# Kernel optimization log

Measured on AMD Instinct MI355X. Metric: run time of the kernel, lower is better.

Reference implementation:

```python
import jax, jax.numpy as jnp
import numpy as np

WBITS = 4
GROUP_SIZE = 64
QMAX = 2 ** WBITS - 1  # 15
EPS = 1e-5


def setup_inputs() -> dict:
    key = jax.random.key(0)
    k1, k2, k3 = jax.random.split(key, 3)
    x = jax.random.normal(k1, (1, 512, 11008), dtype=jnp.float32)
    weight = jax.random.normal(k2, (4096, 11008), dtype=jnp.float32) * 0.02
    bias = jax.random.normal(k3, (4096,), dtype=jnp.float32) * 0.02
    return {"x": x, "weight": weight, "bias": bias}


def fake_quant_groupwise(w: jnp.ndarray) -> jnp.ndarray:
    """Uniform affine (asymmetric) group-wise fake quantization of the weight.

    Groups of GROUP_SIZE contiguous elements along the flattened weight share
    one (scale, zero_point) pair, computed dynamically from min/max per group,
    as in UniformAffineQuantizer(wbits, group_size, weight).
    """
    orig_shape = w.shape
    wg = w.reshape(-1, GROUP_SIZE)                     # [n_groups, G]
    xmin = jnp.min(wg, axis=1, keepdims=True)          # [n_groups, 1]
    xmax = jnp.max(wg, axis=1, keepdims=True)
    scale = jnp.maximum(xmax - xmin, EPS) / QMAX       # [n_groups, 1]
    zero_point = jnp.round(-xmin / scale)              # [n_groups, 1]
    w_int = jnp.clip(jnp.round(wg / scale) + zero_point, 0, QMAX)
    w_dq = (w_int - zero_point) * scale
    return w_dq.reshape(orig_shape)


def reference(x, weight, bias):
    w_q = fake_quant_groupwise(weight)                 # [out, in]
    # F.linear: x @ w_q.T + bias
    out = jnp.einsum('bsi,oi->bso', x, w_q) + bias
    return out
```

## Files before the change

kernel.cpp:

```cpp
#include <hip/hip_runtime.h>
#include <hip/hip_bf16.h>
#include <stdint.h>

typedef __attribute__((ext_vector_type(8))) short bf16x8;
typedef __attribute__((ext_vector_type(8))) short short8;
typedef __attribute__((ext_vector_type(4))) float f32x4;

#define M_DIM 512
#define N_DIM 4096
#define K_DIM 11008
#define KSTEPS 172

#define GLOBAL_AS(p) ((const __attribute__((address_space(1))) void*)(p))
#define LDS_AS(p)    ((__attribute__((address_space(3))) void*)(p))

__device__ __forceinline__ short f2bf(float f) {
    unsigned u = __float_as_uint(f);
    unsigned r = u + 0x7fff + ((u >> 16) & 1);
    return (short)(r >> 16);
}

__device__ __forceinline__ unsigned cvt_pk_bf16(float lo, float hi) {
    unsigned r;
    asm("v_cvt_pk_bf16_f32 %0, %1, %2" : "=v"(r) : "v"(lo), "v"(hi));
    return r;
}

__device__ __forceinline__ float dpp_xor1(float v) {
    return __int_as_float(__builtin_amdgcn_mov_dpp(__float_as_int(v), 0xB1, 0xf, 0xf, true));
}
__device__ __forceinline__ float dpp_xor2(float v) {
    return __int_as_float(__builtin_amdgcn_mov_dpp(__float_as_int(v), 0x4E, 0xf, 0xf, true));
}

__device__ __forceinline__ void fence_bar() {
    asm volatile("" ::: "memory");
    __builtin_amdgcn_s_barrier();
    asm volatile("" ::: "memory");
}
#define LGKM0() asm volatile("s_waitcnt lgkmcnt(0)" ::: "memory")
#define VMCNT(n) asm volatile("s_waitcnt vmcnt(" #n ")" ::: "memory")

__global__ __launch_bounds__(256) void conv_x(const float* __restrict__ x, short* __restrict__ xb) {
    const long long total = (long long)M_DIM * K_DIM;
    for (long long e0 = ((long long)blockIdx.x * 256 + threadIdx.x) * 8;
         e0 < total;
         e0 += (long long)gridDim.x * 256 * 8) {
        const float4* p = (const float4*)(x + e0);
        float4 v0 = p[0];
        float4 v1 = p[1];
        short8 s;
        s[0] = f2bf(v0.x); s[1] = f2bf(v0.y); s[2] = f2bf(v0.z); s[3] = f2bf(v0.w);
        s[4] = f2bf(v1.x); s[5] = f2bf(v1.y); s[6] = f2bf(v1.z); s[7] = f2bf(v1.w);
        *(short8*)(xb + e0) = s;
    }
}

__global__ __launch_bounds__(256, 2) void gemm_fq(const short* __restrict__ A,
                                                  const float* __restrict__ W,
                                                  unsigned short* __restrict__ P,
                                                  int spb) {
    __shared__ short As[2][256 * 64];
    __shared__ short Bs[128 * 64];
    const int tid  = threadIdx.x;
    const int lane = tid & 63;
    const int w    = tid >> 6;
    const int wr   = w >> 1;
    const int wc   = w & 1;
    const int m0   = blockIdx.y * 256;
    const int n0   = blockIdx.x * 128;
    const int kt0  = blockIdx.z * spb;
    const int kt1  = min(kt0 + spb, KSTEPS);

    const int srow = lane >> 3;
    const int sswz = (lane & 7) ^ srow;
    const int rC   = tid >> 2;
    const int qC   = tid & 3;
    const int arow = wr * 128 + (lane & 15);
    const int brow = wc * 64 + (lane & 15);
    const int qb   = lane >> 4;

    f32x4  acc[8][4] = {};
    float4 C0[4], C1[4];

    auto stageA = [&](int d, int kt) {
        #pragma unroll
        for (int i = 0; i < 8; ++i) {
            const int rb = w * 64 + i * 8;
            __builtin_amdgcn_global_load_lds(
                GLOBAL_AS(A + (size_t)(m0 + rb + srow) * K_DIM + kt * 64 + sswz * 8),
                LDS_AS(&As[d][rb * 64]), 16, 0, 0);
        }
    };
    auto loadC = [&](float4 (&dst)[4], int c, int kt) {
        const float4* src = (const float4*)(W + (size_t)(n0 + c * 64 + rC) * K_DIM + (size_t)kt * 64 + qC * 16);
        #pragma unroll
        for (int j = 0; j < 4; ++j) dst[j] = src[j];
    };
    auto quantC = [&](const float4 (&v)[4], int c) {
        const float* pv = (const float*)&v[0];
        float mns[8], mxs[8];
        #pragma unroll
        for (int j = 0; j < 8; ++j) {
            mns[j] = fminf(pv[2 * j], pv[2 * j + 1]);
            mxs[j] = fmaxf(pv[2 * j], pv[2 * j + 1]);
        }
        #pragma unroll
        for (int st = 4; st >= 1; st >>= 1)
            #pragma unroll
            for (int j = 0; j < st; ++j) {
                mns[j] = fminf(mns[j], mns[j + st]);
                mxs[j] = fmaxf(mxs[j], mxs[j + st]);
            }
        float mn = fminf(mns[0], dpp_xor1(mns[0]));
        mn = fminf(mn, dpp_xor2(mn));
        float mx = fmaxf(mxs[0], dpp_xor1(mxs[0]));
        mx = fmaxf(mx, dpp_xor2(mx));
        float range = fmaxf(mx - mn, 1e-5f);
        float scale = range * (1.0f / 15.0f);
        float rs    = 1.0f / scale;
        const int r    = c * 64 + rC;
        const int base = r * 64;
        #pragma unroll
        for (int s4 = 0; s4 < 2; ++s4) {
            float q[8];
            #pragma unroll
            for (int j = 0; j < 8; ++j)
                q[j] = rintf(pv[s4 * 8 + j] * rs) * scale;
            union { unsigned u[4]; short8 s; } pk;
            #pragma unroll
            for (int j = 0; j < 4; ++j)
                pk.u[j] = cvt_pk_bf16(q[2 * j], q[2 * j + 1]);
            const int s = qC * 2 + s4;
            *(short8*)&Bs[base + ((s ^ (r & 7)) * 8)] = pk.s;
        }
    };

    loadC(C0, 0, kt0);
    loadC(C1, 1, kt0);
    stageA(0, kt0);
    VMCNT(12); quantC(C0, 0);
    VMCNT(8);  quantC(C1, 1);
    loadC(C0, 0, kt0 + 1);
    loadC(C1, 1, kt0 + 1);
    VMCNT(8);
    LGKM0();
    fence_bar();

    int par = 0;
    for (int t = kt0; t < kt1; ++t) {
        const int tn  = (t + 1 < kt1) ? t + 1 : t;
        const int tn2 = (t + 2 < kt1) ? t + 2 : kt1 - 1;
        const short* Asc = As[par];

        stageA(par ^ 1, tn);

        bf16x8 bfr[2][4];
        #pragma unroll
        for (int ks = 0; ks < 2; ++ks)
            #pragma unroll
            for (int fn = 0; fn < 4; ++fn) {
                const int r = brow + fn * 16;
                bfr[ks][fn] = *(const bf16x8*)&Bs[r * 64 + (((ks * 4 + qb) ^ (r & 7)) * 8)];
            }
        #pragma unroll
        for (int qd = 0; qd < 4; ++qd) {
            bf16x8 af[2][2];
            #pragma unroll
            for (int ks = 0; ks < 2; ++ks)
                #pragma unroll
                for (int j = 0; j < 2; ++j) {
                    const int r = arow + (qd * 2 + j) * 16;
                    af[ks][j] = *(const bf16x8*)&Asc[r * 64 + (((ks * 4 + qb) ^ (r & 7)) * 8)];
                }
            #pragma unroll
            for (int ks = 0; ks < 2; ++ks)
                #pragma unroll
                for (int j = 0; j < 2; ++j)
                    #pragma unroll
                    for (int fn = 0; fn < 4; ++fn)
                        acc[qd * 2 + j][fn] = __builtin_amdgcn_mfma_f32_16x16x32_bf16(
                            af[ks][j], bfr[ks][fn], acc[qd * 2 + j][fn], 0, 0, 0);
        }
        fence_bar();

        VMCNT(12);
        quantC(C0, 0);
        VMCNT(8);
        quantC(C1, 1);
        loadC(C0, 0, tn2);
        loadC(C1, 1, tn2);
        VMCNT(8);
        LGKM0();
        fence_bar();
        par ^= 1;
    }

    VMCNT(0);

    unsigned short* out = P + (size_t)blockIdx.z * M_DIM * N_DIM;
    #pragma unroll
    for (int fm = 0; fm < 8; ++fm) {
        #pragma unroll
        for (int fn = 0; fn < 4; ++fn) {
            const int col  = n0 + wc * 64 + fn * 16 + (lane & 15);
            const int rowb = m0 + wr * 128 + fm * 16 + (lane >> 4) * 4;
            #pragma unroll
            for (int r = 0; r < 4; ++r) {
                out[(size_t)(rowb + r) * N_DIM + col] = (unsigned short)f2bf(acc[fm][fn][r]);
            }
        }
    }
}

__global__ __launch_bounds__(256) void reduce_out(const unsigned short* __restrict__ P,
                                                  const float* __restrict__ bias,
                                                  float* __restrict__ out,
                                                  int splitk) {
    const size_t total = (size_t)M_DIM * N_DIM;
    for (size_t idx8 = ((size_t)blockIdx.x * 256 + threadIdx.x) * 8;
         idx8 < total;
         idx8 += (size_t)gridDim.x * 256 * 8) {
        const int col = (int)(idx8 % N_DIM);
        float s[8];
        {
            float4 b0 = *(const float4*)(bias + col);
            float4 b1 = *(const float4*)(bias + col + 4);
            s[0] = b0.x; s[1] = b0.y; s[2] = b0.z; s[3] = b0.w;
            s[4] = b1.x; s[5] = b1.y; s[6] = b1.z; s[7] = b1.w;
        }
        for (int sp = 0; sp < splitk; ++sp) {
            short8 p = *(const short8*)(P + (size_t)sp * total + idx8);
            #pragma unroll
            for (int j = 0; j < 8; ++j)
                s[j] += __uint_as_float(((unsigned)(unsigned short)p[j]) << 16);
        }
        float4 o0 = {s[0], s[1], s[2], s[3]};
        float4 o1 = {s[4], s[5], s[6], s[7]};
        *(float4*)(out + idx8) = o0;
        *(float4*)(out + idx8 + 4) = o1;
    }
}

extern "C" void kernel_launch(void* const* d_in, const int* in_sizes, int n_in,
                              void* d_out, int out_size, void* d_ws, size_t ws_size,
                              hipStream_t stream) {
    const float* x    = (const float*)d_in[0];
    const float* wgt  = (const float*)d_in[1];
    const float* bias = (const float*)d_in[2];
    float* out = (float*)d_out;

    char* ws = (char*)d_ws;
    const size_t xb_bytes = (size_t)M_DIM * K_DIM * 2;
    short* xb = (short*)ws;
    unsigned short* part = (unsigned short*)(ws + xb_bytes);

    const size_t per_split = (size_t)M_DIM * N_DIM * 2;
    size_t avail = (ws_size > xb_bytes) ? (ws_size - xb_bytes) : 0;
    int splitk = 1, spb = KSTEPS;
    for (int sk = 8; sk >= 1; --sk) {
        if ((size_t)sk * per_split > avail) continue;
        int s = (KSTEPS + sk - 1) / sk;
        int last = KSTEPS - (sk - 1) * s;
        if (last < 2) continue;
        splitk = sk; spb = s;
        break;
    }

    hipLaunchKernelGGL(conv_x, dim3(2048), dim3(256), 0, stream, x, xb);
    hipLaunchKernelGGL(gemm_fq, dim3(N_DIM / 128, M_DIM / 256, splitk), dim3(256), 0, stream,
                       xb, wgt, part, spb);
    hipLaunchKernelGGL(reduce_out, dim3(1024), dim3(256), 0, stream, part, bias, out, splitk);
}
```

Baseline: 87.97 us.

## Double GEMM block to 512 threads, halving per-wave accumulator tiles

The GEMM block grows from 4 to 8 waves while keeping the same 256x128 output tile. Each wave now computes a 64x64 subtile with half the accumulators, and each thread loads and quantizes one 64-float weight group instead of two. The inner loop is reordered to load B fragments per k-substep. The aim is lower register pressure and more waves to hide latency, at the cost of fewer MFMAs per LDS read and heavier barrier synchronization. The reduce kernel grid is also doubled.

```diff
diff --git a/kernel.cpp b/kernel.cpp
--- a/kernel.cpp
+++ b/kernel.cpp
@@ -56,7 +56,7 @@
     }
 }
 
-__global__ __launch_bounds__(256, 2) void gemm_fq(const short* __restrict__ A,
+__global__ __launch_bounds__(512, 4) void gemm_fq(const short* __restrict__ A,
                                                   const float* __restrict__ W,
                                                   unsigned short* __restrict__ P,
                                                   int spb) {
@@ -76,29 +76,29 @@
     const int sswz = (lane & 7) ^ srow;
     const int rC   = tid >> 2;
     const int qC   = tid & 3;
-    const int arow = wr * 128 + (lane & 15);
+    const int arow = wr * 64 + (lane & 15);
     const int brow = wc * 64 + (lane & 15);
     const int qb   = lane >> 4;
 
-    f32x4  acc[8][4] = {};
-    float4 C0[4], C1[4];
+    f32x4  acc[4][4] = {};
+    float4 C[4];
 
     auto stageA = [&](int d, int kt) {
         #pragma unroll
-        for (int i = 0; i < 8; ++i) {
-            const int rb = w * 64 + i * 8;
+        for (int i = 0; i < 4; ++i) {
+            const int rb = (w * 4 + i) * 8;
             __builtin_amdgcn_global_load_lds(
                 GLOBAL_AS(A + (size_t)(m0 + rb + srow) * K_DIM + kt * 64 + sswz * 8),
                 LDS_AS(&As[d][rb * 64]), 16, 0, 0);
         }
     };
-    auto loadC = [&](float4 (&dst)[4], int c, int kt) {
-        const float4* src = (const float4*)(W + (size_t)(n0 + c * 64 + rC) * K_DIM + (size_t)kt * 64 + qC * 16);
-        #pragma unroll
-        for (int j = 0; j < 4; ++j) dst[j] = src[j];
+    auto loadC = [&](int kt) {
+        const float4* src = (const float4*)(W + (size_t)(n0 + rC) * K_DIM + (size_t)kt * 64 + qC * 16);
+        #pragma unroll
+        for (int j = 0; j < 4; ++j) C[j] = src[j];
     };
-    auto quantC = [&](const float4 (&v)[4], int c) {
-        const float* pv = (const float*)&v[0];
+    auto quantC = [&]() {
+        const float* pv = (const float*)&C[0];
         float mns[8], mxs[8];
         #pragma unroll
         for (int j = 0; j < 8; ++j) {
@@ -119,8 +119,7 @@
         float range = fmaxf(mx - mn, 1e-5f);
         float scale = range * (1.0f / 15.0f);
         float rs    = 1.0f / scale;
-        const int r    = c * 64 + rC;
-        const int base = r * 64;
+        const int base = rC * 64;
         #pragma unroll
         for (int s4 = 0; s4 < 2; ++s4) {
             float q[8];
@@ -132,18 +131,15 @@
             for (int j = 0; j < 4; ++j)
                 pk.u[j] = cvt_pk_bf16(q[2 * j], q[2 * j + 1]);
             const int s = qC * 2 + s4;
-            *(short8*)&Bs[base + ((s ^ (r & 7)) * 8)] = pk.s;
+            *(short8*)&Bs[base + ((s ^ (rC & 7)) * 8)] = pk.s;
         }
     };
 
-    loadC(C0, 0, kt0);
-    loadC(C1, 1, kt0);
+    loadC(kt0);
     stageA(0, kt0);
-    VMCNT(12); quantC(C0, 0);
-    VMCNT(8);  quantC(C1, 1);
-    loadC(C0, 0, kt0 + 1);
-    loadC(C1, 1, kt0 + 1);
-    VMCNT(8);
+    VMCNT(4);  quantC();
+    loadC(kt0 + 1);
+    VMCNT(4);
     LGKM0();
     fence_bar();
 
@@ -155,42 +151,30 @@
 
         stageA(par ^ 1, tn);
 
-        bf16x8 bfr[2][4];
-        #pragma unroll
-        for (int ks = 0; ks < 2; ++ks)
+        #pragma unroll
+        for (int ks = 0; ks < 2; ++ks) {
+            bf16x8 bfr[4];
             #pragma unroll
             for (int fn = 0; fn < 4; ++fn) {
                 const int r = brow + fn * 16;
-                bfr[ks][fn] = *(const bf16x8*)&Bs[r * 64 + (((ks * 4 + qb) ^ (r & 7)) * 8)];
-            }
-        #pragma unroll
-        for (int qd = 0; qd < 4; ++qd) {
-            bf16x8 af[2][2];
-            #pragma unroll
-            for (int ks = 0; ks < 2; ++ks)
+                bfr[fn] = *(const bf16x8*)&Bs[r * 64 + (((ks * 4 + qb) ^ (r & 7)) * 8)];
+            }
+            #pragma unroll
+            for (int fm = 0; fm < 4; ++fm) {
+                const int r = arow + fm * 16;
+                bf16x8 af = *(const bf16x8*)&Asc[r * 64 + (((ks * 4 + qb) ^ (r & 7)) * 8)];
                 #pragma unroll
-                for (int j = 0; j < 2; ++j) {
-                    const int r = arow + (qd * 2 + j) * 16;
-                    af[ks][j] = *(const bf16x8*)&Asc[r * 64 + (((ks * 4 + qb) ^ (r & 7)) * 8)];
-                }
-            #pragma unroll
-            for (int ks = 0; ks < 2; ++ks)
-                #pragma unroll
-                for (int j = 0; j < 2; ++j)
-                    #pragma unroll
-                    for (int fn = 0; fn < 4; ++fn)
-                        acc[qd * 2 + j][fn] = __builtin_amdgcn_mfma_f32_16x16x32_bf16(
-                            af[ks][j], bfr[ks][fn], acc[qd * 2 + j][fn], 0, 0, 0);
+                for (int fn = 0; fn < 4; ++fn)
+                    acc[fm][fn] = __builtin_amdgcn_mfma_f32_16x16x32_bf16(
+                        af, bfr[fn], acc[fm][fn], 0, 0, 0);
+            }
         }
         fence_bar();
 
-        VMCNT(12);
-        quantC(C0, 0);
-        VMCNT(8);
-        quantC(C1, 1);
-        loadC(C0, 0, tn2);
-        loadC(C1, 1, tn2);
-        VMCNT(8);
+        VMCNT(4);
+        quantC();
+        loadC(tn2);
+        VMCNT(4);
         LGKM0();
         fence_bar();
         par ^= 1;
@@ -200,11 +184,11 @@
 
     unsigned short* out = P + (size_t)blockIdx.z * M_DIM * N_DIM;
     #pragma unroll
-    for (int fm = 0; fm < 8; ++fm) {
+    for (int fm = 0; fm < 4; ++fm) {
         #pragma unroll
         for (int fn = 0; fn < 4; ++fn) {
             const int col  = n0 + wc * 64 + fn * 16 + (lane & 15);
-            const int rowb = m0 + wr * 128 + fm * 16 + (lane >> 4) * 4;
+            const int rowb = m0 + wr * 64 + fm * 16 + (lane >> 4) * 4;
             #pragma unroll
             for (int r = 0; r < 4; ++r) {
                 out[(size_t)(rowb + r) * N_DIM + col] = (unsigned short)f2bf(acc[fm][fn][r]);
@@ -268,7 +252,7 @@
     }
 
     hipLaunchKernelGGL(conv_x, dim3(2048), dim3(256), 0, stream, x, xb);
-    hipLaunchKernelGGL(gemm_fq, dim3(N_DIM / 128, M_DIM / 256, splitk), dim3(256), 0, stream,
+    hipLaunchKernelGGL(gemm_fq, dim3(N_DIM / 128, M_DIM / 256, splitk), dim3(512), 0, stream,
                        xb, wgt, part, spb);
-    hipLaunchKernelGGL(reduce_out, dim3(1024), dim3(256), 0, stream, part, bias, out, splitk);
-}
+    hipLaunchKernelGGL(reduce_out, dim3(2048), dim3(256), 0, stream, part, bias, out, splitk);
+}
```

Result: no change. 87.95 us, median of 3 (-0.0%).
